# Kernel optimization log

Hardware: AMD Instinct MI355X
Metric: run time of the kernel (lower is better)

Reference implementation:

```python
import jax, jax.numpy as jnp
import numpy as np

A = 3                      # anchors per location
HS = [256, 128, 64, 32]    # square feature-map sizes (FPN levels)
B = 4                      # batch (num images)
SIZES = [A * h * h for h in HS]
T = sum(SIZES)             # 261120 anchors per image
PRE_N, POST_N = 512, 512
NMS_TH, SCORE_TH, MIN_SIZE = 0.7, 0.0, 1e-3
LOG_MAX = 4.135166556742356   # log(1000/16), standard delta clamp
MAXV = 8                      # max vertices of quad-quad intersection
LVL_OFF = 8192.0              # per-level coordinate offset for batched NMS


def box_corners(b):
    # b: [..., 5] (cx, cy, w, h, angle) -> [..., 4, 2] CCW corners
    cx, cy, w, h, a = (b[..., i] for i in range(5))
    c, s = jnp.cos(a), jnp.sin(a)
    dx = 0.5 * jnp.stack([w, -w, -w, w], -1)
    dy = 0.5 * jnp.stack([h, h, -h, -h], -1)
    x = cx[..., None] + dx * c[..., None] - dy * s[..., None]
    y = cy[..., None] + dx * s[..., None] + dy * c[..., None]
    return jnp.stack([x, y], -1)


def _clip(poly, cnt, p1, p2):
    # Sutherland-Hodgman clip of poly (padded [MAXV,2], cnt valid) by half-plane left of p1->p2
    e = p2 - p1
    d = e[0] * (poly[:, 1] - p1[1]) - e[1] * (poly[:, 0] - p1[0])
    def body(carry, i):
        out, oc = carry
        nxt = jnp.where(i + 1 < cnt, i + 1, 0)
        cur_in, nxt_in = d[i] >= 0, d[nxt] >= 0
        valid = i < cnt
        keep = valid & cur_in
        out = out.at[oc].set(jnp.where(keep, poly[i], out[oc]))
        oc = oc + keep.astype(jnp.int32)
        crs = valid & (cur_in != nxt_in)
        den = d[i] - d[nxt]
        t = d[i] / jnp.where(den == 0, 1.0, den)
        ip = poly[i] + t * (poly[nxt] - poly[i])
        out = out.at[oc].set(jnp.where(crs, ip, out[oc]))
        oc = oc + crs.astype(jnp.int32)
        return (out, oc), None
    (out, oc), _ = jax.lax.scan(body, (jnp.zeros((MAXV, 2), poly.dtype), jnp.int32(0)), jnp.arange(MAXV))
    return out, oc


def _inter_area(ca, cb):
    # intersection area of two convex quads given CCW corners [4,2]
    poly = jnp.zeros((MAXV, 2), ca.dtype).at[:4].set(ca)
    cnt = jnp.int32(4)
    for k in range(4):
        poly, cnt = _clip(poly, cnt, cb[k], cb[(k + 1) % 4])
    i = jnp.arange(MAXV)
    nxt = jnp.where(i + 1 < cnt, i + 1, 0)
    cr = poly[i, 0] * poly[nxt, 1] - poly[nxt, 0] * poly[i, 1]
    area = 0.5 * jnp.abs(jnp.sum(jnp.where(i < cnt, cr, 0.0)))
    return jnp.where(cnt >= 3, area, 0.0)


def decode(deltas, anchors):
    # XYWHA decode with 6-dim deltas (dx,dy,dw,dh,dsin,dcos), weights all 1.0
    ax, ay, aw, ah, aa = (anchors[..., i] for i in range(5))
    dx, dy, dw, dh, ds, dc = (deltas[..., i] for i in range(6))
    dw = jnp.minimum(dw, LOG_MAX)
    dh = jnp.minimum(dh, LOG_MAX)
    return jnp.stack([ax + dx * aw, ay + dy * ah, aw * jnp.exp(dw),
                      ah * jnp.exp(dh), aa + jnp.arctan2(ds, dc)], -1)


def nms_image(boxes, scores, levels):
    # boxes [N,5], scores [N] (post-sigmoid), levels [N] int32 -> fixed-size padded outputs
    N = scores.shape[0]
    valid = (boxes[:, 2] >= MIN_SIZE) & (boxes[:, 3] >= MIN_SIZE) & (scores >= SCORE_TH)
    s = jnp.where(valid, scores, -jnp.inf)
    order = jnp.argsort(-s)
    bx, sc, vd = boxes[order], s[order], valid[order]
    off = levels[order].astype(bx.dtype) * LVL_OFF
    nb = bx.at[:, :2].add(off[:, None])          # level offset => cross-level IoU == 0
    nbg = jax.lax.stop_gradient(nb)
    corners = box_corners(nbg)                    # [N,4,2]
    areas = nbg[:, 2] * nbg[:, 3]
    CH = 128
    def chunk_fn(args):
        cc, ca = args
        def row(ci, ai):
            inter = jax.vmap(lambda cj: _inter_area(ci, cj))(corners)
            return inter / (ai + areas - inter + 1e-7)
        return jax.vmap(row)(cc, ca)
    iou = jax.lax.map(chunk_fn, (corners.reshape(N // CH, CH, 4, 2),
                                 areas.reshape(N // CH, CH))).reshape(N, N)
    idx = jnp.arange(N)
    def body(i, sup):
        keep_i = ~sup[i]
        return sup | (keep_i & (iou[i] > NMS_TH) & (idx > i))
    sup = jax.lax.fori_loop(0, N, body, ~vd)      # invalid boxes start suppressed
    kept = ~sup
    _, top_i = jax.lax.top_k(jnp.where(kept, sc, -jnp.inf), POST_N)
    ok = kept[top_i]
    return jnp.where(ok[:, None], bx[top_i], 0.0), jnp.where(ok, sc[top_i], 0.0)


def rpn_forward(objs, dlts, anchors):
    obj_f, dlt_f = [], []
    for o, d, h in zip(objs, dlts, HS):
        # permute_and_flatten: [B,A,H,W] -> [B,H*W*A]; [B,A*6,H,W] -> [B,H*W*A,6]
        obj_f.append(o.transpose(0, 2, 3, 1).reshape(B, -1))
        dlt_f.append(d.reshape(B, A, 6, h, h).transpose(0, 3, 4, 1, 2).reshape(B, -1, 6))
    objectness = jnp.concatenate(obj_f, 1)        # [B, T]
    deltas = jnp.concatenate(dlt_f, 1)            # [B, T, 6]
    proposals = decode(deltas, anchors)           # [B, T, 5]
    parts, offset = [], 0
    for sz in SIZES:                               # per-level top-k
        k = min(PRE_N, sz)
        _, ti = jax.lax.top_k(objectness[:, offset:offset + sz], k)
        parts.append(ti + offset)
        offset += sz
    top_idx = jnp.concatenate(parts, 1)           # [B, 4*PRE_N]
    levels = jnp.concatenate([jnp.full((sz,), i, jnp.int32) for i, sz in enumerate(SIZES)])
    obj_top = jnp.take_along_axis(objectness, top_idx, 1)
    prop_top = jnp.take_along_axis(proposals, top_idx[..., None], 1)
    lvl_top = levels[top_idx]
    scores = jax.nn.sigmoid(obj_top)
    return jax.vmap(nms_image)(prop_top, scores, lvl_top)


def setup_inputs() -> dict:
    key = jax.random.key(0)
    ks = jax.random.split(key, 9)
    inp = {}
    for i, h in enumerate(HS):
        inp[f"obj{i}"] = jax.random.normal(ks[i], (B, A, h, h), jnp.float32)
        inp[f"dlt{i}"] = 0.25 * jax.random.normal(ks[4 + i], (B, A * 6, h, h), jnp.float32)
    u = jax.random.uniform(ks[8], (B, T, 5), jnp.float32)
    inp["anchors"] = jnp.stack([u[..., 0] * 1024.0, u[..., 1] * 1024.0,
                                8.0 + 120.0 * u[..., 2], 8.0 + 120.0 * u[..., 3],
                                jnp.pi * (u[..., 4] - 0.5)], -1)
    return inp


def reference(obj0, obj1, obj2, obj3, dlt0, dlt1, dlt2, dlt3, anchors):
    # returns (boxes [B, POST_N, 5], scores [B, POST_N]) padded with zeros
    return rpn_forward([obj0, obj1, obj2, obj3], [dlt0, dlt1, dlt2, dlt3], anchors)
```

## Files before the change

kernel.cpp:

```cpp
#include <hip/hip_runtime.h>

typedef unsigned int u32;
typedef unsigned long long u64;
typedef unsigned char u8;

#define NB 4
#define T_ANCH 261120
#define NCAND 2048
#define KSEL 512
#define POSTN 512
#define LOG_MAXF 4.135166556742356f
#define NMS_TH 0.7f
#define LVL_OFF_F 8192.0f
#define BINS 4096
#define EQCAP 8192
#define PAIR_CAP (1u<<20)
#define K4A_BLOCKS 2048
#define K4A_ROWS 4
#define K1_BLOCKS 256

__device__ __forceinline__ u32 mono32(float f){
  u32 u = __float_as_uint(f);
  return (u & 0x80000000u) ? ~u : (u | 0x80000000u);
}
__device__ __forceinline__ int lvl_hw(int lvl){ return 65536 >> (2*lvl); }
__device__ __forceinline__ int lvl_off(int lvl){
  return (lvl>0?196608:0) + (lvl>1?49152:0) + (lvl>2?12288:0);
}
__device__ __forceinline__ void k1_map(int bx, int& b, int& lvl, int& ch){
  b = bx >> 6;
  int c = bx & 63;
  if (c < 48){ lvl = 0; ch = c; }
  else if (c < 60){ lvl = 1; ch = c - 48; }
  else if (c < 63){ lvl = 2; ch = c - 60; }
  else { lvl = 3; ch = 0; }
}

__global__ __launch_bounds__(1024) void k1a_hist(
    const float* __restrict__ o0, const float* __restrict__ o1,
    const float* __restrict__ o2, const float* __restrict__ o3,
    u32* __restrict__ ghist)
{
  int b, lvl, ch;
  k1_map(blockIdx.x, b, lvl, ch);
  const float* ob = (lvl==0)?o0 : (lvl==1)?o1 : (lvl==2)?o2 : o3;
  int hw = lvl_hw(lvl);
  int size = 3*hw;
  int n4 = size >> 2;
  int i4 = ch*1024 + threadIdx.x;
  __shared__ u32 hist[BINS];
  for (int i = threadIdx.x; i < BINS; i += 1024) hist[i] = 0;
  __syncthreads();
  if (i4 < n4){
    float4 v = ((const float4*)(ob + (size_t)b*size))[i4];
    atomicAdd(&hist[mono32(v.x) >> 20], 1u);
    atomicAdd(&hist[mono32(v.y) >> 20], 1u);
    atomicAdd(&hist[mono32(v.z) >> 20], 1u);
    atomicAdd(&hist[mono32(v.w) >> 20], 1u);
  }
  __syncthreads();
  u32* out = ghist + (size_t)blockIdx.x*BINS;
  for (int i = threadIdx.x; i < BINS; i += 1024) out[i] = hist[i];
}

__global__ __launch_bounds__(1024) void k1b_thresh(
    const u32* __restrict__ ghist, u32* __restrict__ gb0,
    u32* __restrict__ gcA, u32* __restrict__ emitcnt, u32* __restrict__ tiecnt)
{
  int bid = blockIdx.x;
  int b = bid >> 2, lvl = bid & 3;
  int base_bx = b*64 + (lvl==0?0 : lvl==1?48 : lvl==2?60 : 63);
  int nch = (lvl==0?48 : lvl==1?12 : lvl==2?3 : 1);
  __shared__ u32 hist[BINS];
  __shared__ u32 coarse[64];
  int t = threadIdx.x;
  u32 c0=0,c1=0,c2=0,c3=0;
  for (int ch = 0; ch < nch; ++ch){
    const u32* h = ghist + (size_t)(base_bx+ch)*BINS;
    c0 += h[4*t+0]; c1 += h[4*t+1]; c2 += h[4*t+2]; c3 += h[4*t+3];
  }
  hist[4*t+0]=c0; hist[4*t+1]=c1; hist[4*t+2]=c2; hist[4*t+3]=c3;
  __syncthreads();
  if (t < 64){
    u32 s = 0;
    for (int z = 0; z < 64; ++z) s += hist[t*64 + z];
    coarse[t] = s;
  }
  __syncthreads();
  if (t == 0){
    u32 acc = 0;
    int cb = 63;
    while (acc + coarse[cb] < (u32)KSEL){ acc += coarse[cb]; --cb; }
    int z = cb*64 + 63;
    while (acc + hist[z] < (u32)KSEL){ acc += hist[z]; --z; }
    gb0[bid] = (u32)z;
    gcA[bid] = acc;
    emitcnt[bid] = 0;
    tiecnt[bid] = 0;
  }
}

__global__ __launch_bounds__(1024) void k1c_classify(
    const float* __restrict__ o0, const float* __restrict__ o1,
    const float* __restrict__ o2, const float* __restrict__ o3,
    const u32* __restrict__ gb0,
    u32* __restrict__ emitcnt, u32* __restrict__ tiecnt,
    int* __restrict__ cand_j, u64* __restrict__ gtie)
{
  int b, lvl, ch;
  k1_map(blockIdx.x, b, lvl, ch);
  int bid16 = b*4 + lvl;
  const float* ob = (lvl==0)?o0 : (lvl==1)?o1 : (lvl==2)?o2 : o3;
  int hw = lvl_hw(lvl);
  int size = 3*hw;
  int n4 = size >> 2;
  int i4 = ch*1024 + threadIdx.x;

  __shared__ u32 dbuf[KSEL];
  __shared__ u64 tbuf[4096];
  __shared__ u32 dn, tn, dbase, tbase;
  if (threadIdx.x == 0){ dn = 0; tn = 0; }
  __syncthreads();

  u32 b0v = gb0[bid16];
  if (i4 < n4){
    float4 v = ((const float4*)(ob + (size_t)b*size))[i4];
    int L = i4 << 2;
    int a = L / hw;
    int pix = L - a*hw;
    int j0 = pix*3 + a;
    float vv[4] = {v.x, v.y, v.z, v.w};
    #pragma unroll
    for (int q = 0; q < 4; ++q){
      u32 m = mono32(vv[q]);
      u32 bin = m >> 20;
      int j = j0 + 3*q;
      if (bin > b0v){
        u32 s = atomicAdd(&dn, 1u);
        if (s < (u32)KSEL) dbuf[s] = (u32)j;
      } else if (bin == b0v){
        u32 s = atomicAdd(&tn, 1u);
        if (s < 4096u) tbuf[s] = ((u64)m << 32) | (u32)(~(u32)j);
      }
    }
  }
  __syncthreads();
  if (threadIdx.x == 0){
    dbase = dn ? atomicAdd(&emitcnt[bid16], dn) : 0u;
    tbase = tn ? atomicAdd(&tiecnt[bid16], tn) : 0u;
  }
  __syncthreads();
  for (u32 x = threadIdx.x; x < dn; x += 1024){
    u32 s = dbase + x;
    if (s < (u32)KSEL) cand_j[bid16*KSEL + s] = (int)dbuf[x];
  }
  for (u32 x = threadIdx.x; x < tn; x += 1024){
    u32 s = tbase + x;
    if (s < (u32)EQCAP) gtie[(size_t)bid16*EQCAP + s] = tbuf[x];
  }
}

__global__ __launch_bounds__(1024) void k1d_tie(
    const u64* __restrict__ gtie, const u32* __restrict__ tiecnt,
    const u32* __restrict__ gcA, u32* __restrict__ emitcnt,
    int* __restrict__ cand_j)
{
  int bid = blockIdx.x;
  __shared__ u64 eq[EQCAP];
  __shared__ u32 wbuf[KSEL];
  __shared__ u32 wn, wbase;
  u32 n = tiecnt[bid]; if (n > (u32)EQCAP) n = (u32)EQCAP;
  u32 k = (u32)KSEL - gcA[bid];
  if (threadIdx.x == 0) wn = 0;
  for (u32 i = threadIdx.x; i < n; i += 1024) eq[i] = gtie[(size_t)bid*EQCAP + i];
  __syncthreads();
  for (u32 i = threadIdx.x; i < n; i += 1024){
    u64 ki = eq[i];
    u32 r = 0;
    for (u32 m = 0; m < n; ++m) r += (eq[m] > ki) ? 1u : 0u;
    if (r < k){
      u32 s = atomicAdd(&wn, 1u);
      if (s < (u32)KSEL) wbuf[s] = (u32)(~(u32)ki);
    }
  }
  __syncthreads();
  if (threadIdx.x == 0) wbase = wn ? atomicAdd(&emitcnt[bid], wn) : 0u;
  __syncthreads();
  for (u32 x = threadIdx.x; x < wn; x += 1024){
    u32 s = wbase + x;
    if (s < (u32)KSEL) cand_j[bid*KSEL + s] = (int)wbuf[x];
  }
}

__global__ __launch_bounds__(256) void k2_decode(
    const float* __restrict__ o0, const float* __restrict__ o1,
    const float* __restrict__ o2, const float* __restrict__ o3,
    const float* __restrict__ d0, const float* __restrict__ d1,
    const float* __restrict__ d2, const float* __restrict__ d3,
    const float* __restrict__ anchors,
    const int* __restrict__ cand_j,
    float* __restrict__ cscore, u32* __restrict__ csmono,
    u64* __restrict__ ctb, float* __restrict__ cbox, u8* __restrict__ cvalid)
{
  int c = blockIdx.x*256 + threadIdx.x;
  if (c >= NB*NCAND) return;
  int pair = c >> 9;
  int b = pair >> 2, lvl = pair & 3;
  int j = cand_j[c];
  int hw = lvl_hw(lvl);
  u32 pix = (u32)j / 3u;
  u32 a = (u32)j - pix*3u;
  const float* ob = (lvl==0)?o0 : (lvl==1)?o1 : (lvl==2)?o2 : o3;
  const float* dl = (lvl==0)?d0 : (lvl==1)?d1 : (lvl==2)?d2 : d3;

  float ov = ob[(size_t)(b*3 + (int)a)*hw + pix];
  size_t dbase = ((size_t)(b*3 + (int)a)*6)*(size_t)hw + pix;
  float dx  = dl[dbase + 0*(size_t)hw];
  float dy  = dl[dbase + 1*(size_t)hw];
  float dw  = dl[dbase + 2*(size_t)hw];
  float dh  = dl[dbase + 3*(size_t)hw];
  float dsn = dl[dbase + 4*(size_t)hw];
  float dcs = dl[dbase + 5*(size_t)hw];
  int tt = lvl_off(lvl) + j;
  const float* an = anchors + ((size_t)b*T_ANCH + tt)*5;
  float ax=an[0], ay=an[1], aw=an[2], ah=an[3], aa=an[4];
  dw = fminf(dw, LOG_MAXF); dh = fminf(dh, LOG_MAXF);
  float cx = ax + dx*aw;
  float cy = ay + dy*ah;
  float w  = aw * expf(dw);
  float h  = ah * expf(dh);
  float ang = aa + atan2f(dsn, dcs);
  double sd = 1.0 / (1.0 + exp(-(double)ov));
  float sc = (float)sd;
  bool valid = (w >= 1e-3f) && (h >= 1e-3f) && (sc >= 0.0f);
  cscore[c] = sc;
  csmono[c] = valid ? mono32(sc) : 0u;
  ctb[c] = ((u64)lvl << 50) | ((u64)(u32)(~mono32(ov)) << 18) | (u64)(u32)j;
  cvalid[c] = valid ? 1 : 0;
  float* bb = cbox + (size_t)c*5;
  bb[0]=cx; bb[1]=cy; bb[2]=w; bb[3]=h; bb[4]=ang;
}

__global__ __launch_bounds__(256) void k3_rank(
    const u32* __restrict__ csmono, const u64* __restrict__ ctb,
    const float* __restrict__ cscore, const float* __restrict__ cbox,
    const u8* __restrict__ cvalid,
    float* __restrict__ sscore, float* __restrict__ sbox,
    float* __restrict__ geom, float4* __restrict__ aabb4,
    u8* __restrict__ svalid)
{
  int b   = blockIdx.x >> 6;
  int blk = blockIdx.x & 63;
  __shared__ u32 sm[NCAND];
  __shared__ u64 stb[NCAND];
  __shared__ u32 cnt[32][8];
  for (int k = threadIdx.x; k < NCAND; k += 256){
    sm[k]  = csmono[b*NCAND + k];
    stb[k] = ctb[b*NCAND + k];
  }
  __syncthreads();
  int esub = threadIdx.x >> 3;
  int ssub = threadIdx.x & 7;
  int id = blk*32 + esub;
  u32 ms = sm[id];
  u64 mt = stb[id];
  u32 r = 0;
  #pragma unroll 8
  for (int it = 0; it < 256; ++it){
    int m = it*8 + ssub;
    u32 s2 = sm[m]; u64 t2 = stb[m];
    r += ((s2 > ms) || (s2 == ms && t2 < mt)) ? 1u : 0u;
  }
  cnt[esub][ssub] = r;
  __syncthreads();
  if (ssub == 0){
    u32 rank = 0;
    #pragma unroll
    for (int q = 0; q < 8; ++q) rank += cnt[esub][q];
    int gsrc = b*NCAND + id;
    int gdst = b*NCAND + (int)rank;
    sscore[gdst] = cscore[gsrc];
    svalid[gdst] = cvalid[gsrc];
    float b0 = cbox[(size_t)gsrc*5+0], b1 = cbox[(size_t)gsrc*5+1];
    float b2 = cbox[(size_t)gsrc*5+2], b3 = cbox[(size_t)gsrc*5+3];
    float b4 = cbox[(size_t)gsrc*5+4];
    float* sb = sbox + (size_t)gdst*5;
    sb[0]=b0; sb[1]=b1; sb[2]=b2; sb[3]=b3; sb[4]=b4;
    int lvl = (int)((mt >> 50) & 3ull);
    float offv = (float)lvl * LVL_OFF_F;
    float cx = b0 + offv, cy = b1 + offv, w=b2, h=b3, ang=b4;
    float cc = cosf(ang), sn = sinf(ang);
    float hx = 0.5f*w, hy = 0.5f*h;
    float x0 = cx + hx*cc - hy*sn, y0 = cy + hx*sn + hy*cc;
    float x1 = cx - hx*cc - hy*sn, y1 = cy - hx*sn + hy*cc;
    float x2 = cx - hx*cc + hy*sn, y2 = cy - hx*sn - hy*cc;
    float x3 = cx + hx*cc + hy*sn, y3 = cy + hx*sn - hy*cc;
    float minx = fminf(fminf(x0,x1),fminf(x2,x3));
    float maxx = fmaxf(fmaxf(x0,x1),fmaxf(x2,x3));
    float miny = fminf(fminf(y0,y1),fminf(y2,y3));
    float maxy = fmaxf(fmaxf(y0,y1),fmaxf(y2,y3));
    float* g = geom + (size_t)gdst*16;
    g[0]=minx; g[1]=maxx; g[2]=miny; g[3]=maxy; g[4]=w*h;
    g[5]=x0; g[6]=y0; g[7]=x1; g[8]=y1; g[9]=x2; g[10]=y2; g[11]=x3; g[12]=y3;
    aabb4[gdst] = make_float4(minx, maxx, miny, maxy);
  }
}

__global__ __launch_bounds__(256) void k4a_aabb(
    const float4* __restrict__ aabb4,
    u32* __restrict__ list, u32* __restrict__ gcount)
{
  __shared__ u32 lbuf[K4A_ROWS*NCAND];
  __shared__ u32 lcnt, lbase;
  if (threadIdx.x == 0) lcnt = 0;
  __syncthreads();
  int img = blockIdx.x >> 9;
  int i0  = (blockIdx.x & 511) * K4A_ROWS;
  #pragma unroll
  for (int r = 0; r < K4A_ROWS; ++r){
    int i = i0 + r;
    float4 gi = aabb4[img*NCAND + i];
    for (int j = threadIdx.x; j < NCAND; j += 256){
      bool pass = false;
      if (j > i){
        float4 gj = aabb4[img*NCAND + j];
        pass = !(gi.x > gj.y || gj.x > gi.y || gi.z > gj.w || gj.z > gi.w);
      }
      if (pass){
        u32 s = atomicAdd(&lcnt, 1u);
        lbuf[s] = (u32)((img << 22) | (i << 11) | j);
      }
    }
  }
  __syncthreads();
  if (threadIdx.x == 0) lbase = lcnt ? atomicAdd(gcount, lcnt) : 0u;
  __syncthreads();
  u32 n = lcnt, bs = lbase;
  for (u32 x = threadIdx.x; x < n; x += 256){
    u32 idx = bs + x;
    if (idx < PAIR_CAP) list[idx] = lbuf[x];
  }
}

__device__ __forceinline__ void emit_pt(float* ox, float* oy, int oc, float x, float y){
  #pragma unroll
  for (int s = 0; s < 8; ++s) if (s == oc){ ox[s] = x; oy[s] = y; }
}

__device__ float quad_inter(const float* ca, const float* cb){
  float px[8], py[8];
  #pragma unroll
  for (int q = 0; q < 8; ++q){ px[q]=0.f; py[q]=0.f; }
  #pragma unroll
  for (int q = 0; q < 4; ++q){ px[q]=ca[2*q]; py[q]=ca[2*q+1]; }
  int cnt = 4;
  #pragma unroll
  for (int e = 0; e < 4; ++e){
    float p1x = cb[2*e],         p1y = cb[2*e+1];
    float p2x = cb[(2*e+2)&7],   p2y = cb[(2*e+3)&7];
    float ex = p2x-p1x, ey = p2y-p1y;
    float d[8];
    #pragma unroll
    for (int q = 0; q < 8; ++q) d[q] = ex*(py[q]-p1y) - ey*(px[q]-p1x);
    float ox[8], oy[8];
    #pragma unroll
    for (int q = 0; q < 8; ++q){ ox[q]=0.f; oy[q]=0.f; }
    int oc = 0;
    #pragma unroll
    for (int q = 0; q < 8; ++q){
      if (q < cnt){
        bool last = (q+1 >= cnt);
        float dn  = last ? d[0]  : d[(q+1)&7];
        bool in0 = (d[q] >= 0.0f), in1 = (dn >= 0.0f);
        if (in0){ emit_pt(ox,oy,oc,px[q],py[q]); oc++; }
        if (in0 != in1){
          float pnx = last ? px[0] : px[(q+1)&7];
          float pny = last ? py[0] : py[(q+1)&7];
          float den = d[q] - dn;
          float t = d[q] / ((den == 0.0f) ? 1.0f : den);
          emit_pt(ox,oy,oc, px[q] + t*(pnx-px[q]), py[q] + t*(pny-py[q]));
          oc++;
        }
      }
    }
    cnt = (oc > 8) ? 8 : oc;
    #pragma unroll
    for (int q = 0; q < 8; ++q){ px[q]=ox[q]; py[q]=oy[q]; }
  }
  if (cnt < 3) return 0.0f;
  float s = 0.0f;
  #pragma unroll
  for (int q = 0; q < 8; ++q){
    if (q < cnt){
      bool last = (q+1 >= cnt);
      float pnx = last ? px[0] : px[(q+1)&7];
      float pny = last ? py[0] : py[(q+1)&7];
      s += px[q]*pny - pnx*py[q];
    }
  }
  return 0.5f*fabsf(s);
}

__global__ __launch_bounds__(256) void k4b_clip(
    const float* __restrict__ geom, const u32* __restrict__ list,
    const u32* __restrict__ gcount, u64* __restrict__ mask,
    u64* __restrict__ rowflag)
{
  u32 count = *gcount;
  if (count > PAIR_CAP) count = PAIR_CAP;
  for (u32 idx = blockIdx.x*256 + threadIdx.x; idx < count; idx += gridDim.x*256){
    u32 gt = list[idx];
    int img = (int)(gt >> 22);
    int rem = (int)(gt & ((1u<<22)-1));
    int i = rem >> 11;
    int j = rem & (NCAND-1);
    const float* gi = geom + ((size_t)(img*NCAND + i))*16;
    const float* gj = geom + ((size_t)(img*NCAND + j))*16;
    float inter = quad_inter(gi+5, gj+5);
    float iou = inter / (gi[4] + gj[4] - inter + 1e-7f);
    if (iou > NMS_TH){
      atomicOr(&mask[((size_t)(img*NCAND + i))*32 + (j >> 6)], 1ull << (j & 63));
      atomicOr(&rowflag[(size_t)img*32 + (i >> 6)], 1ull << (i & 63));
    }
  }
}

__global__ __launch_bounds__(1024) void k5_nms_out(
    const u64* __restrict__ mask, const u64* __restrict__ rowflag,
    const u8* __restrict__ svalid,
    const float* __restrict__ sbox, const float* __restrict__ sscore,
    float* __restrict__ out)
{
  int b = blockIdx.x;
  __shared__ u32 fid[NCAND];
  __shared__ u32 wcnt[32], wpref[32];
  __shared__ u64 s_kept[32];
  __shared__ u32 pref[32];
  __shared__ u32 s_F;
  int t = threadIdx.x;
  int wid = t >> 6, lane = t & 63;

  if (t < 32) wcnt[t] = (u32)__popcll(rowflag[b*32 + t]);
  __syncthreads();
  if (t == 0){
    u32 run = 0;
    for (int w = 0; w < 32; ++w){ wpref[w] = run; run += wcnt[w]; }
    s_F = run;
  }
  __syncthreads();
  if (t < 32){
    u64 fw = rowflag[b*32 + t];
    u32 o = wpref[t];
    while (fw){
      int bpos = __builtin_ctzll(fw);
      fid[o++] = (u32)(t*64 + bpos);
      fw &= fw - 1;
    }
  }
  for (int x = t; x < POSTN*5; x += 1024) out[(size_t)b*POSTN*5 + x] = 0.0f;
  for (int x = t; x < POSTN;   x += 1024) out[(size_t)NB*POSTN*5 + b*POSTN + x] = 0.0f;
  __syncthreads();

  if (wid == 0){
    u32 slo = 0, shi = 0;
    {
      int wl = lane & 31;
      u64 w = 0;
      for (int q = 0; q < 64; ++q)
        if (!svalid[b*NCAND + wl*64 + q]) w |= (1ull << q);
      slo = (u32)w; shi = (u32)(w >> 32);
    }
    u32 F = s_F;
    const u64* mb = mask + ((size_t)b*NCAND)*32;
    for (u32 f = 0; f < F; f += 8){
      u32 myfid = 0;
      if (f + (lane & 7) < F) myfid = fid[f + (lane & 7)];
      u64 v[8];
      #pragma unroll
      for (int q = 0; q < 8; ++q){
        if (f + q < F){
          u32 fq = (u32)__builtin_amdgcn_readlane((int)myfid, q);
          v[q] = mb[(size_t)fq*32 + (lane & 31)];
        } else v[q] = 0ull;
      }
      #pragma unroll
      for (int q = 0; q < 8; ++q){
        if (f + q < F){
          u32 i = (u32)__builtin_amdgcn_readlane((int)myfid, q);
          int wi = (int)(i >> 6);
          u32 wlo = (u32)__builtin_amdgcn_readlane((int)slo, wi);
          u32 whi = (u32)__builtin_amdgcn_readlane((int)shi, wi);
          u64 w = ((u64)whi << 32) | wlo;
          u32 keep = (u32)((~w >> (i & 63)) & 1ull);
          u64 vm = v[q] & (0ull - (u64)keep);
          slo |= (u32)vm; shi |= (u32)(vm >> 32);
        }
      }
    }
    if (lane < 32) s_kept[lane] = ~(((u64)shi << 32) | slo);
  }
  __syncthreads();

  if (t < 32) pref[t] = (u32)__popcll(s_kept[t]);
  __syncthreads();
  if (t == 0){
    u32 run = 0;
    for (int w = 0; w < 32; ++w){ u32 tv = pref[w]; pref[w] = run; run += tv; }
  }
  __syncthreads();
  for (int i = t; i < NCAND; i += 1024){
    u64 kw = s_kept[i >> 6];
    if ((kw >> (i & 63)) & 1ull){
      u32 rank = pref[i >> 6] + (u32)__popcll(kw & ((1ull << (i & 63)) - 1ull));
      if (rank < POSTN){
        const float* bp = sbox + ((size_t)(b*NCAND + i))*5;
        float* op = out + ((size_t)(b*POSTN + rank))*5;
        op[0]=bp[0]; op[1]=bp[1]; op[2]=bp[2]; op[3]=bp[3]; op[4]=bp[4];
        out[(size_t)NB*POSTN*5 + b*POSTN + rank] = sscore[b*NCAND + i];
      }
    }
  }
}

extern "C" void kernel_launch(void* const* d_in, const int* in_sizes, int n_in,
                              void* d_out, int out_size, void* d_ws, size_t ws_size,
                              hipStream_t stream)
{
  (void)out_size; (void)ws_size;
  const float *obj[4] = {nullptr,nullptr,nullptr,nullptr};
  const float *dlt[4] = {nullptr,nullptr,nullptr,nullptr};
  const float *anchors = nullptr;
  for (int i = 0; i < n_in; ++i){
    int s = in_sizes[i];
    const float* p = (const float*)d_in[i];
    switch (s){
      case 786432:  obj[0] = p; break;
      case 4718592: dlt[0] = p; break;
      case 196608:  obj[1] = p; break;
      case 1179648: dlt[1] = p; break;
      case 49152:   obj[2] = p; break;
      case 294912:  dlt[2] = p; break;
      case 12288:   obj[3] = p; break;
      case 73728:   dlt[3] = p; break;
      case 5222400: anchors = p; break;
      default: break;
    }
  }

  char* wsb = (char*)d_ws;
  size_t off = 0;
  auto alloc = [&](size_t bytes)->void*{
    size_t cur = (off + 255) & ~(size_t)255;
    off = cur + bytes;
    return (void*)(wsb + cur);
  };
  int*   cand_j = (int*)  alloc(16*KSEL*sizeof(int));
  float* cscore = (float*)alloc((size_t)NB*NCAND*sizeof(float));
  u32*   csmono = (u32*)  alloc((size_t)NB*NCAND*sizeof(u32));
  u64*   ctb    = (u64*)  alloc((size_t)NB*NCAND*sizeof(u64));
  float* cbox   = (float*)alloc((size_t)NB*NCAND*5*sizeof(float));
  u8*    cvalid = (u8*)   alloc((size_t)NB*NCAND);
  float* sscore = (float*)alloc((size_t)NB*NCAND*sizeof(float));
  float* sbox   = (float*)alloc((size_t)NB*NCAND*5*sizeof(float));
  u8*    svalid = (u8*)   alloc((size_t)NB*NCAND);
  float* geom   = (float*)alloc((size_t)NB*NCAND*16*sizeof(float));
  float4* aabb4 = (float4*)alloc((size_t)NB*NCAND*sizeof(float4));
  size_t mask_bytes = (size_t)NB*NCAND*32*sizeof(u64);
  u64*   maskp  = (u64*)  alloc(mask_bytes);
  u64*   rowflag= (u64*)  alloc((size_t)NB*32*sizeof(u64));
  u32*   pcount = (u32*)  alloc(sizeof(u32));
  u32*   plist  = (u32*)  alloc((size_t)PAIR_CAP*sizeof(u32));
  u32*   ghist  = (u32*)  alloc((size_t)K1_BLOCKS*BINS*sizeof(u32));
  u64*   gtie   = (u64*)  alloc((size_t)16*EQCAP*sizeof(u64));
  u32*   gb0    = (u32*)  alloc(16*sizeof(u32));
  u32*   gcA    = (u32*)  alloc(16*sizeof(u32));
  u32*   emitc  = (u32*)  alloc(16*sizeof(u32));
  u32*   tiec   = (u32*)  alloc(16*sizeof(u32));

  hipMemsetAsync(maskp, 0, mask_bytes + (size_t)NB*32*sizeof(u64) + 256, stream);

  hipLaunchKernelGGL(k1a_hist, dim3(K1_BLOCKS), dim3(1024), 0, stream,
                     obj[0], obj[1], obj[2], obj[3], ghist);
  hipLaunchKernelGGL(k1b_thresh, dim3(16), dim3(1024), 0, stream,
                     ghist, gb0, gcA, emitc, tiec);
  hipLaunchKernelGGL(k1c_classify, dim3(K1_BLOCKS), dim3(1024), 0, stream,
                     obj[0], obj[1], obj[2], obj[3], gb0, emitc, tiec,
                     cand_j, gtie);
  hipLaunchKernelGGL(k1d_tie, dim3(16), dim3(1024), 0, stream,
                     gtie, tiec, gcA, emitc, cand_j);
  hipLaunchKernelGGL(k2_decode, dim3(32), dim3(256), 0, stream,
                     obj[0], obj[1], obj[2], obj[3],
                     dlt[0], dlt[1], dlt[2], dlt[3],
                     anchors, cand_j, cscore, csmono, ctb, cbox, cvalid);
  hipLaunchKernelGGL(k3_rank, dim3(256), dim3(256), 0, stream,
                     csmono, ctb, cscore, cbox, cvalid, sscore, sbox, geom,
                     aabb4, svalid);
  hipLaunchKernelGGL(k4a_aabb, dim3(K4A_BLOCKS), dim3(256), 0, stream,
                     aabb4, plist, pcount);
  hipLaunchKernelGGL(k4b_clip, dim3(256), dim3(256), 0, stream,
                     geom, plist, pcount, maskp, rowflag);
  hipLaunchKernelGGL(k5_nms_out, dim3(4), dim3(1024), 0, stream,
                     maskp, rowflag, svalid, sbox, sscore, (float*)d_out);
}
```

Measured before the change: 201.2 us.

## Fuse top-k selection stages with last-block-done tickets, merging five kernels into two

The histogram and threshold kernels become one: blocks atomically merge their histograms into per-(image, level) global bins, and the last block to arrive, found by a ticket counter, computes the threshold. Classify, tie resolution and decode are fused the same way, so the last block per group resolves ties and decodes that group's 512 candidates. This removes three kernel launches and their serial gaps, and shrinks the global histogram buffer. In exchange it adds global atomics, threadfences and coherent atomic reads, and the tie and decode work now runs on only 16 blocks of 1024 threads.

```diff
diff --git a/kernel.cpp b/kernel.cpp
--- a/kernel.cpp
+++ b/kernel.cpp
@@ -35,21 +35,30 @@
   else if (c < 63){ lvl = 2; ch = c - 60; }
   else { lvl = 3; ch = 0; }
 }
-
-__global__ __launch_bounds__(1024) void k1a_hist(
+__device__ __forceinline__ u32 coh_read32(u32* p){ return atomicAdd(p, 0u); }
+__device__ __forceinline__ u64 coh_read64(u64* p){ return atomicAdd((unsigned long long*)p, 0ull); }
+
+__global__ __launch_bounds__(1024) void kA_hist_thresh(
     const float* __restrict__ o0, const float* __restrict__ o1,
     const float* __restrict__ o2, const float* __restrict__ o3,
-    u32* __restrict__ ghist)
+    u32* __restrict__ ghist16, u32* __restrict__ ticket,
+    u32* __restrict__ gb0, u32* __restrict__ gcA,
+    u32* __restrict__ emitcnt, u32* __restrict__ tiecnt)
 {
   int b, lvl, ch;
   k1_map(blockIdx.x, b, lvl, ch);
+  int bid16 = b*4 + lvl;
+  int nch = (lvl==0?48 : lvl==1?12 : lvl==2?3 : 1);
   const float* ob = (lvl==0)?o0 : (lvl==1)?o1 : (lvl==2)?o2 : o3;
   int hw = lvl_hw(lvl);
   int size = 3*hw;
   int n4 = size >> 2;
   int i4 = ch*1024 + threadIdx.x;
   __shared__ u32 hist[BINS];
-  for (int i = threadIdx.x; i < BINS; i += 1024) hist[i] = 0;
+  __shared__ u32 coarse[64];
+  __shared__ u32 s_old;
+  int t = threadIdx.x;
+  for (int i = t; i < BINS; i += 1024) hist[i] = 0;
   __syncthreads();
   if (i4 < n4){
     float4 v = ((const float4*)(ob + (size_t)b*size))[i4];
@@ -59,27 +68,17 @@
     atomicAdd(&hist[mono32(v.w) >> 20], 1u);
   }
   __syncthreads();
-  u32* out = ghist + (size_t)blockIdx.x*BINS;
-  for (int i = threadIdx.x; i < BINS; i += 1024) out[i] = hist[i];
-}
-
-__global__ __launch_bounds__(1024) void k1b_thresh(
-    const u32* __restrict__ ghist, u32* __restrict__ gb0,
-    u32* __restrict__ gcA, u32* __restrict__ emitcnt, u32* __restrict__ tiecnt)
-{
-  int bid = blockIdx.x;
-  int b = bid >> 2, lvl = bid & 3;
-  int base_bx = b*64 + (lvl==0?0 : lvl==1?48 : lvl==2?60 : 63);
-  int nch = (lvl==0?48 : lvl==1?12 : lvl==2?3 : 1);
-  __shared__ u32 hist[BINS];
-  __shared__ u32 coarse[64];
-  int t = threadIdx.x;
-  u32 c0=0,c1=0,c2=0,c3=0;
-  for (int ch = 0; ch < nch; ++ch){
-    const u32* h = ghist + (size_t)(base_bx+ch)*BINS;
-    c0 += h[4*t+0]; c1 += h[4*t+1]; c2 += h[4*t+2]; c3 += h[4*t+3];
-  }
-  hist[4*t+0]=c0; hist[4*t+1]=c1; hist[4*t+2]=c2; hist[4*t+3]=c3;
+  u32* gh = ghist16 + (size_t)bid16*BINS;
+  for (int i = t; i < BINS; i += 1024){
+    u32 c = hist[i];
+    if (c) atomicAdd(&gh[i], c);
+  }
+  __syncthreads();
+  if (t == 0){ __threadfence(); s_old = atomicAdd(&ticket[bid16], 1u); }
+  __syncthreads();
+  if (s_old != (u32)(nch - 1)) return;
+  __threadfence();
+  for (int i = t; i < BINS; i += 1024) hist[i] = coh_read32(&gh[i]);
   __syncthreads();
   if (t < 64){
     u32 s = 0;
@@ -93,33 +92,43 @@
     while (acc + coarse[cb] < (u32)KSEL){ acc += coarse[cb]; --cb; }
     int z = cb*64 + 63;
     while (acc + hist[z] < (u32)KSEL){ acc += hist[z]; --z; }
-    gb0[bid] = (u32)z;
-    gcA[bid] = acc;
-    emitcnt[bid] = 0;
-    tiecnt[bid] = 0;
-  }
-}
-
-__global__ __launch_bounds__(1024) void k1c_classify(
+    gb0[bid16] = (u32)z;
+    gcA[bid16] = acc;
+    emitcnt[bid16] = 0;
+    tiecnt[bid16] = 0;
+  }
+}
+
+__global__ __launch_bounds__(1024) void kC_classify_tie_decode(
     const float* __restrict__ o0, const float* __restrict__ o1,
     const float* __restrict__ o2, const float* __restrict__ o3,
-    const u32* __restrict__ gb0,
+    const float* __restrict__ d0, const float* __restrict__ d1,
+    const float* __restrict__ d2, const float* __restrict__ d3,
+    const float* __restrict__ anchors,
+    const u32* __restrict__ gb0, const u32* __restrict__ gcA,
     u32* __restrict__ emitcnt, u32* __restrict__ tiecnt,
-    int* __restrict__ cand_j, u64* __restrict__ gtie)
+    u32* __restrict__ ticket2,
+    int* __restrict__ cand_j, u64* __restrict__ gtie,
+    float* __restrict__ cscore, u32* __restrict__ csmono,
+    u64* __restrict__ ctb, float* __restrict__ cbox, u8* __restrict__ cvalid)
 {
   int b, lvl, ch;
   k1_map(blockIdx.x, b, lvl, ch);
   int bid16 = b*4 + lvl;
+  int nch = (lvl==0?48 : lvl==1?12 : lvl==2?3 : 1);
   const float* ob = (lvl==0)?o0 : (lvl==1)?o1 : (lvl==2)?o2 : o3;
+  const float* dl = (lvl==0)?d0 : (lvl==1)?d1 : (lvl==2)?d2 : d3;
   int hw = lvl_hw(lvl);
   int size = 3*hw;
   int n4 = size >> 2;
   int i4 = ch*1024 + threadIdx.x;
-
+  int t = threadIdx.x;
+
+  __shared__ u64 eq[EQCAP];
   __shared__ u32 dbuf[KSEL];
-  __shared__ u64 tbuf[4096];
-  __shared__ u32 dn, tn, dbase, tbase;
-  if (threadIdx.x == 0){ dn = 0; tn = 0; }
+  __shared__ u32 wbuf[KSEL];
+  __shared__ u32 dn, tn, dbase, tbase, s_old, wn, wbase;
+  if (t == 0){ dn = 0; tn = 0; }
   __syncthreads();
 
   u32 b0v = gb0[bid16];
@@ -140,41 +149,38 @@
         if (s < (u32)KSEL) dbuf[s] = (u32)j;
       } else if (bin == b0v){
         u32 s = atomicAdd(&tn, 1u);
-        if (s < 4096u) tbuf[s] = ((u64)m << 32) | (u32)(~(u32)j);
-      }
-    }
-  }
-  __syncthreads();
-  if (threadIdx.x == 0){
+        if (s < 4096u) eq[s] = ((u64)m << 32) | (u32)(~(u32)j);
+      }
+    }
+  }
+  __syncthreads();
+  if (t == 0){
     dbase = dn ? atomicAdd(&emitcnt[bid16], dn) : 0u;
     tbase = tn ? atomicAdd(&tiecnt[bid16], tn) : 0u;
   }
   __syncthreads();
-  for (u32 x = threadIdx.x; x < dn; x += 1024){
+  for (u32 x = t; x < dn; x += 1024){
     u32 s = dbase + x;
     if (s < (u32)KSEL) cand_j[bid16*KSEL + s] = (int)dbuf[x];
   }
-  for (u32 x = threadIdx.x; x < tn; x += 1024){
+  for (u32 x = t; x < tn; x += 1024){
     u32 s = tbase + x;
-    if (s < (u32)EQCAP) gtie[(size_t)bid16*EQCAP + s] = tbuf[x];
-  }
-}
-
-__global__ __launch_bounds__(1024) void k1d_tie(
-    const u64* __restrict__ gtie, const u32* __restrict__ tiecnt,
-    const u32* __restrict__ gcA, u32* __restrict__ emitcnt,
-    int* __restrict__ cand_j)
-{
-  int bid = blockIdx.x;
-  __shared__ u64 eq[EQCAP];
-  __shared__ u32 wbuf[KSEL];
-  __shared__ u32 wn, wbase;
-  u32 n = tiecnt[bid]; if (n > (u32)EQCAP) n = (u32)EQCAP;
-  u32 k = (u32)KSEL - gcA[bid];
-  if (threadIdx.x == 0) wn = 0;
-  for (u32 i = threadIdx.x; i < n; i += 1024) eq[i] = gtie[(size_t)bid*EQCAP + i];
-  __syncthreads();
-  for (u32 i = threadIdx.x; i < n; i += 1024){
+    if (s < (u32)EQCAP) gtie[(size_t)bid16*EQCAP + s] = eq[x];
+  }
+  __syncthreads();
+  if (t == 0){ __threadfence(); s_old = atomicAdd(&ticket2[bid16], 1u); }
+  __syncthreads();
+  if (s_old != (u32)(nch - 1)) return;
+  __threadfence();
+
+  u32 n = coh_read32(&tiecnt[bid16]);
+  if (n > (u32)EQCAP) n = (u32)EQCAP;
+  u32 k = (u32)KSEL - gcA[bid16];
+  if (t == 0) wn = 0;
+  for (u32 i = t; i < n; i += 1024)
+    eq[i] = coh_read64(&gtie[(size_t)bid16*EQCAP + i]);
+  __syncthreads();
+  for (u32 i = t; i < n; i += 1024){
     u64 ki = eq[i];
     u32 r = 0;
     for (u32 m = 0; m < n; ++m) r += (eq[m] > ki) ? 1u : 0u;
@@ -184,61 +190,46 @@
     }
   }
   __syncthreads();
-  if (threadIdx.x == 0) wbase = wn ? atomicAdd(&emitcnt[bid], wn) : 0u;
-  __syncthreads();
-  for (u32 x = threadIdx.x; x < wn; x += 1024){
+  if (t == 0) wbase = wn ? atomicAdd(&emitcnt[bid16], wn) : 0u;
+  __syncthreads();
+  for (u32 x = t; x < wn; x += 1024){
     u32 s = wbase + x;
-    if (s < (u32)KSEL) cand_j[bid*KSEL + s] = (int)wbuf[x];
-  }
-}
-
-__global__ __launch_bounds__(256) void k2_decode(
-    const float* __restrict__ o0, const float* __restrict__ o1,
-    const float* __restrict__ o2, const float* __restrict__ o3,
-    const float* __restrict__ d0, const float* __restrict__ d1,
-    const float* __restrict__ d2, const float* __restrict__ d3,
-    const float* __restrict__ anchors,
-    const int* __restrict__ cand_j,
-    float* __restrict__ cscore, u32* __restrict__ csmono,
-    u64* __restrict__ ctb, float* __restrict__ cbox, u8* __restrict__ cvalid)
-{
-  int c = blockIdx.x*256 + threadIdx.x;
-  if (c >= NB*NCAND) return;
-  int pair = c >> 9;
-  int b = pair >> 2, lvl = pair & 3;
-  int j = cand_j[c];
-  int hw = lvl_hw(lvl);
-  u32 pix = (u32)j / 3u;
-  u32 a = (u32)j - pix*3u;
-  const float* ob = (lvl==0)?o0 : (lvl==1)?o1 : (lvl==2)?o2 : o3;
-  const float* dl = (lvl==0)?d0 : (lvl==1)?d1 : (lvl==2)?d2 : d3;
-
-  float ov = ob[(size_t)(b*3 + (int)a)*hw + pix];
-  size_t dbase = ((size_t)(b*3 + (int)a)*6)*(size_t)hw + pix;
-  float dx  = dl[dbase + 0*(size_t)hw];
-  float dy  = dl[dbase + 1*(size_t)hw];
-  float dw  = dl[dbase + 2*(size_t)hw];
-  float dh  = dl[dbase + 3*(size_t)hw];
-  float dsn = dl[dbase + 4*(size_t)hw];
-  float dcs = dl[dbase + 5*(size_t)hw];
-  int tt = lvl_off(lvl) + j;
-  const float* an = anchors + ((size_t)b*T_ANCH + tt)*5;
-  float ax=an[0], ay=an[1], aw=an[2], ah=an[3], aa=an[4];
-  dw = fminf(dw, LOG_MAXF); dh = fminf(dh, LOG_MAXF);
-  float cx = ax + dx*aw;
-  float cy = ay + dy*ah;
-  float w  = aw * expf(dw);
-  float h  = ah * expf(dh);
-  float ang = aa + atan2f(dsn, dcs);
-  double sd = 1.0 / (1.0 + exp(-(double)ov));
-  float sc = (float)sd;
-  bool valid = (w >= 1e-3f) && (h >= 1e-3f) && (sc >= 0.0f);
-  cscore[c] = sc;
-  csmono[c] = valid ? mono32(sc) : 0u;
-  ctb[c] = ((u64)lvl << 50) | ((u64)(u32)(~mono32(ov)) << 18) | (u64)(u32)j;
-  cvalid[c] = valid ? 1 : 0;
-  float* bb = cbox + (size_t)c*5;
-  bb[0]=cx; bb[1]=cy; bb[2]=w; bb[3]=h; bb[4]=ang;
+    if (s < (u32)KSEL) cand_j[bid16*KSEL + s] = (int)wbuf[x];
+  }
+  __syncthreads();
+
+  for (int c5 = t; c5 < KSEL; c5 += 1024){
+    int c = bid16*KSEL + c5;
+    int j = (int)coh_read32((u32*)&cand_j[c]);
+    u32 pix = (u32)j / 3u;
+    u32 a = (u32)j - pix*3u;
+    float ov = ob[(size_t)(b*3 + (int)a)*hw + pix];
+    size_t dbase2 = ((size_t)(b*3 + (int)a)*6)*(size_t)hw + pix;
+    float dx  = dl[dbase2 + 0*(size_t)hw];
+    float dy  = dl[dbase2 + 1*(size_t)hw];
+    float dw  = dl[dbase2 + 2*(size_t)hw];
+    float dh  = dl[dbase2 + 3*(size_t)hw];
+    float dsn = dl[dbase2 + 4*(size_t)hw];
+    float dcs = dl[dbase2 + 5*(size_t)hw];
+    int tt = lvl_off(lvl) + j;
+    const float* an = anchors + ((size_t)b*T_ANCH + tt)*5;
+    float ax=an[0], ay=an[1], aw=an[2], ah=an[3], aa=an[4];
+    dw = fminf(dw, LOG_MAXF); dh = fminf(dh, LOG_MAXF);
+    float cx = ax + dx*aw;
+    float cy = ay + dy*ah;
+    float w  = aw * expf(dw);
+    float h  = ah * expf(dh);
+    float ang = aa + atan2f(dsn, dcs);
+    double sd = 1.0 / (1.0 + exp(-(double)ov));
+    float sc = (float)sd;
+    bool valid = (w >= 1e-3f) && (h >= 1e-3f) && (sc >= 0.0f);
+    cscore[c] = sc;
+    csmono[c] = valid ? mono32(sc) : 0u;
+    ctb[c] = ((u64)lvl << 50) | ((u64)(u32)(~mono32(ov)) << 18) | (u64)(u32)j;
+    cvalid[c] = valid ? 1 : 0;
+    float* bb = cbox + (size_t)c*5;
+    bb[0]=cx; bb[1]=cy; bb[2]=w; bb[3]=h; bb[4]=ang;
+  }
 }
 
 __global__ __launch_bounds__(256) void k3_rank(
@@ -565,33 +556,31 @@
   u8*    svalid = (u8*)   alloc((size_t)NB*NCAND);
   float* geom   = (float*)alloc((size_t)NB*NCAND*16*sizeof(float));
   float4* aabb4 = (float4*)alloc((size_t)NB*NCAND*sizeof(float4));
-  size_t mask_bytes = (size_t)NB*NCAND*32*sizeof(u64);
-  u64*   maskp  = (u64*)  alloc(mask_bytes);
-  u64*   rowflag= (u64*)  alloc((size_t)NB*32*sizeof(u64));
-  u32*   pcount = (u32*)  alloc(sizeof(u32));
-  u32*   plist  = (u32*)  alloc((size_t)PAIR_CAP*sizeof(u32));
-  u32*   ghist  = (u32*)  alloc((size_t)K1_BLOCKS*BINS*sizeof(u32));
   u64*   gtie   = (u64*)  alloc((size_t)16*EQCAP*sizeof(u64));
   u32*   gb0    = (u32*)  alloc(16*sizeof(u32));
   u32*   gcA    = (u32*)  alloc(16*sizeof(u32));
   u32*   emitc  = (u32*)  alloc(16*sizeof(u32));
   u32*   tiec   = (u32*)  alloc(16*sizeof(u32));
-
-  hipMemsetAsync(maskp, 0, mask_bytes + (size_t)NB*32*sizeof(u64) + 256, stream);
-
-  hipLaunchKernelGGL(k1a_hist, dim3(K1_BLOCKS), dim3(1024), 0, stream,
-                     obj[0], obj[1], obj[2], obj[3], ghist);
-  hipLaunchKernelGGL(k1b_thresh, dim3(16), dim3(1024), 0, stream,
-                     ghist, gb0, gcA, emitc, tiec);
-  hipLaunchKernelGGL(k1c_classify, dim3(K1_BLOCKS), dim3(1024), 0, stream,
-                     obj[0], obj[1], obj[2], obj[3], gb0, emitc, tiec,
-                     cand_j, gtie);
-  hipLaunchKernelGGL(k1d_tie, dim3(16), dim3(1024), 0, stream,
-                     gtie, tiec, gcA, emitc, cand_j);
-  hipLaunchKernelGGL(k2_decode, dim3(32), dim3(256), 0, stream,
+  u32*   plist  = (u32*)  alloc((size_t)PAIR_CAP*sizeof(u32));
+  size_t zero_start = (off + 255) & ~(size_t)255;
+  u64*   maskp  = (u64*)  alloc((size_t)NB*NCAND*32*sizeof(u64));
+  u64*   rowflag= (u64*)  alloc((size_t)NB*32*sizeof(u64));
+  u32*   pcount = (u32*)  alloc(sizeof(u32));
+  u32*   ghist16= (u32*)  alloc((size_t)16*BINS*sizeof(u32));
+  u32*   ticket = (u32*)  alloc(16*sizeof(u32));
+  u32*   ticket2= (u32*)  alloc(16*sizeof(u32));
+  size_t zero_bytes = off - zero_start;
+
+  hipMemsetAsync(wsb + zero_start, 0, zero_bytes, stream);
+
+  hipLaunchKernelGGL(kA_hist_thresh, dim3(K1_BLOCKS), dim3(1024), 0, stream,
+                     obj[0], obj[1], obj[2], obj[3],
+                     ghist16, ticket, gb0, gcA, emitc, tiec);
+  hipLaunchKernelGGL(kC_classify_tie_decode, dim3(K1_BLOCKS), dim3(1024), 0, stream,
                      obj[0], obj[1], obj[2], obj[3],
                      dlt[0], dlt[1], dlt[2], dlt[3],
-                     anchors, cand_j, cscore, csmono, ctb, cbox, cvalid);
+                     anchors, gb0, gcA, emitc, tiec, ticket2,
+                     cand_j, gtie, cscore, csmono, ctb, cbox, cvalid);
   hipLaunchKernelGGL(k3_rank, dim3(256), dim3(256), 0, stream,
                      csmono, ctb, cscore, cbox, cvalid, sscore, sbox, geom,
                      aabb4, svalid);
```

New measurement: 219.2 us. 8.9% more time.
